# Performance work log

Hardware: AMD Instinct MI355X
Metric: run time of the kernel (lower is better)

The kernel has to match this reference:

```python
import jax, jax.numpy as jnp
import numpy as np

B, C, H, W = 8, 384, 32, 32
NH, DK, DV = 8, 48, 48
CFF = 4 * C
L = H * W
NBIAS = (2 * H - 1) * (2 * W - 1)
LN_EPS = 1e-5


def _relative_indices(height, width):
    # rel_idx[q, k] = (gy_k - gy_q + H) * W + (gx_k - gx_q + W), matching the torch loop
    gy, gx = np.meshgrid(np.arange(height), np.arange(width), indexing='ij')
    gy = gy.ravel(); gx = gx.ravel()
    rel = (gy[None, :] - gy[:, None] + height) * width + (gx[None, :] - gx[:, None] + width)
    return jnp.asarray(rel, dtype=jnp.int64)


def setup_inputs() -> dict:
    key = jax.random.key(0)
    ks = jax.random.split(key, 10)
    s = 0.02  # small init scale
    return {
        'x': jax.random.normal(ks[0], (B, C, H, W), dtype=jnp.float32),
        'gamma': jnp.ones((C,), jnp.float32),
        'beta': jnp.zeros((C,), jnp.float32),
        'Wq': jax.random.normal(ks[1], (NH * DK, C), jnp.float32) * s,
        'Wk': jax.random.normal(ks[2], (NH * DK, C), jnp.float32) * s,
        'Wv': jax.random.normal(ks[3], (NH * DV, C), jnp.float32) * s,
        'Wo': jax.random.normal(ks[4], (C, NH * DV), jnp.float32) * s,
        'bo': jnp.zeros((C,), jnp.float32),
        'rel_bias': jax.random.normal(ks[5], (NH, NBIAS), jnp.float32),
        'fc1_w': jax.random.normal(ks[6], (CFF, C), jnp.float32) * s,
        'fc1_b': jnp.zeros((CFF,), jnp.float32),
        'fc2_w': jax.random.normal(ks[7], (C, CFF), jnp.float32) * s,
        'fc2_b': jnp.zeros((C,), jnp.float32),
        'rel_idx': _relative_indices(H, W),
    }


def reference(x, gamma, beta, Wq, Wk, Wv, Wo, bo, rel_bias,
              fc1_w, fc1_b, fc2_w, fc2_b, rel_idx):
    b, c, h_sp, w_sp = x.shape
    l = h_sp * w_sp
    nh = rel_bias.shape[0]
    dk = Wq.shape[0] // nh
    dv = Wv.shape[0] // nh

    # LayerNorm over channel dim (NHWC), then flatten to tokens [b, l, c]
    t = jnp.transpose(x, (0, 2, 3, 1))
    mu = jnp.mean(t, axis=-1, keepdims=True)
    var = jnp.mean(jnp.square(t - mu), axis=-1, keepdims=True)
    t = (t - mu) / jnp.sqrt(var + LN_EPS) * gamma + beta
    tok = t.reshape(b, l, c)

    q = (tok @ Wq.T).reshape(b, l, nh, dk)
    k = (tok @ Wk.T).reshape(b, l, nh, dk)
    v = (tok @ Wv.T).reshape(b, l, nh, dv)

    # gathered relative position bias: [nh, l, l]
    bias = rel_bias[:, rel_idx]
    # note: original applies NO 1/sqrt(d_k) scaling
    scores = jnp.einsum('blhd,bmhd->bhlm', q, k) + bias[None]
    attn = jax.nn.softmax(scores, axis=-1)
    out = jnp.einsum('bhlm,bmhd->blhd', attn, v).reshape(b, l, nh * dv)
    out = out @ Wo.T + bo  # [b, l, c]
    out = jnp.transpose(out, (0, 2, 1)).reshape(b, c, h_sp, w_sp)

    y = x + out  # attention residual (x_stem = x, no downsampling)

    # FFN: 1x1 convs == per-pixel linear over channels; exact (erf) gelu as torch default
    u = jnp.einsum('bchw,oc->bohw', y, fc1_w) + fc1_b[None, :, None, None]
    u = jax.nn.gelu(u, approximate=False)
    u = jnp.einsum('bchw,oc->bohw', u, fc2_w) + fc2_b[None, :, None, None]
    return y + u
```

## Files before the change

kernel.cpp:

```cpp
#include <hip/hip_runtime.h>
#include <math.h>

#define SL 1024
#define CH 384
#define NHEAD 8
#define DH 48
#define NBIAS 3969
#define NTOK 8192
#define BATCH 8
#define CFF 1536
#define LN_EPS 1e-5f
#define QKVLD 1152
#define HMS 3145728
#define LOG2E 1.4426950408889634f

#define WQKV_OFF 0
#define WO_OFF   442368
#define F1_OFF   589824
#define F2_OFF   1179648
#define WTOT     1769472

typedef float floatx4 __attribute__((ext_vector_type(4)));
typedef short bf16x8 __attribute__((ext_vector_type(8)));

__device__ __forceinline__ unsigned f2bf_u(float f) {
  unsigned u = __float_as_uint(f);
  return (u + 0x7fffu + ((u >> 16) & 1u)) >> 16;
}
__device__ __forceinline__ unsigned pack2(float a, float b) {
  return f2bf_u(a) | (f2bf_u(b) << 16);
}
__device__ __forceinline__ float bf2f(short s) {
  return __uint_as_float(((unsigned)(unsigned short)s) << 16);
}

__device__ __forceinline__ void gload_lds16(const void* g, void* l) {
  __builtin_amdgcn_global_load_lds(
      (const __attribute__((address_space(1))) void*)g,
      (__attribute__((address_space(3))) void*)l, 16, 0, 0);
}

__global__ void k_w2bf(const float* __restrict__ Wq, const float* __restrict__ Wk,
                       const float* __restrict__ Wv, const float* __restrict__ Wo,
                       const float* __restrict__ f1, const float* __restrict__ f2,
                       short* __restrict__ dst) {
  size_t i = ((size_t)blockIdx.x * 256 + threadIdx.x) * 8;
  if (i >= WTOT) return;
  const float* s;
  size_t base;
  if (i < 147456)        { s = Wq; base = 0; }
  else if (i < 294912)   { s = Wk; base = 147456; }
  else if (i < WO_OFF)   { s = Wv; base = 294912; }
  else if (i < F1_OFF)   { s = Wo; base = WO_OFF; }
  else if (i < F2_OFF)   { s = f1; base = F1_OFF; }
  else                   { s = f2; base = F2_OFF; }
  const float4* p = (const float4*)(s + (i - base));
  float4 a = p[0], b = p[1];
  uint4 o;
  o.x = pack2(a.x, a.y); o.y = pack2(a.z, a.w);
  o.z = pack2(b.x, b.y); o.w = pack2(b.z, b.w);
  *(uint4*)(dst + i) = o;
}

__global__ __launch_bounds__(256) void k_ln_fused(
    const float* __restrict__ x, const float* __restrict__ gamma,
    const float* __restrict__ beta, short* __restrict__ tok) {
  __shared__ float sx[32][385];
  int b = blockIdx.y, l0 = blockIdx.x * 32;
  int tid = threadIdx.x;
  const float* xb = x + (size_t)b * CH * SL;
  int cr = tid >> 3, ls = (tid & 7) * 4;
#pragma unroll
  for (int c0 = 0; c0 < CH; c0 += 32) {
    int c = c0 + cr;
    float4 v = *(const float4*)(xb + (size_t)c * SL + l0 + ls);
    sx[ls + 0][c] = v.x; sx[ls + 1][c] = v.y;
    sx[ls + 2][c] = v.z; sx[ls + 3][c] = v.w;
  }
  __syncthreads();
  int tl = tid >> 3, p = tid & 7;
  float vals[48];
  float s = 0.f, q = 0.f;
#pragma unroll
  for (int i = 0; i < 48; i++) {
    float v = sx[tl][p * 48 + i];
    vals[i] = v; s += v; q += v * v;
  }
  s += __shfl_xor(s, 1, 64); q += __shfl_xor(q, 1, 64);
  s += __shfl_xor(s, 2, 64); q += __shfl_xor(q, 2, 64);
  s += __shfl_xor(s, 4, 64); q += __shfl_xor(q, 4, 64);
  float mu = s * (1.0f / CH);
  float rstd = rsqrtf(q * (1.0f / CH) - mu * mu + LN_EPS);
  short* orow = tok + (size_t)(b * SL + l0 + tl) * CH + p * 48;
#pragma unroll
  for (int i = 0; i < 48; i += 2) {
    float a = (vals[i] - mu) * rstd * gamma[p * 48 + i] + beta[p * 48 + i];
    float c = (vals[i + 1] - mu) * rstd * gamma[p * 48 + i + 1] + beta[p * 48 + i + 1];
    *(unsigned*)(orow + i) = pack2(a, c);
  }
}

template <int BM, bool GELU, bool HAS_BIAS, int RES_MODE, int OUT_MODE>
__global__ __launch_bounds__(256) void k_gemm_mfma(
    const short* __restrict__ A, const short* __restrict__ W,
    const float* __restrict__ bias, const float* __restrict__ res,
    float* __restrict__ Cf, short* __restrict__ Cb, float* __restrict__ Ct,
    short* __restrict__ Chm, int N, int K) {
  constexpr int MI = BM / 32;
  constexpr int ASI = BM * 2 / 64;
  __shared__ short As[BM * 64];
  __shared__ short Bs[128 * 64];
  int tid = threadIdx.x;
  int wid = tid >> 6, lane = tid & 63;
  int lanelo = lane & 15, quad = lane >> 4;
  int wm = wid & 1, wn = wid >> 1;
  int m0 = blockIdx.y * BM, n0 = blockIdx.x * 128;

  const short* Aga[ASI];
  short* Ala[ASI];
#pragma unroll
  for (int s = 0; s < ASI; s++) {
    int p = wid * (BM * 2) + s * 64 + lane;
    int row = p >> 3, ch = (p & 7) ^ (row & 7);
    Aga[s] = A + (size_t)(m0 + row) * K + ch * 8;
    Ala[s] = As + (wid * (BM * 2) + s * 64) * 8;
  }
  const short* Bga[4];
  short* Bla[4];
#pragma unroll
  for (int s = 0; s < 4; s++) {
    int p = wid * 256 + s * 64 + lane;
    int row = p >> 3, ch = (p & 7) ^ (row & 7);
    Bga[s] = W + (size_t)(n0 + row) * K + ch * 8;
    Bla[s] = Bs + (wid * 256 + s * 64) * 8;
  }

  floatx4 acc[MI][4];
#pragma unroll
  for (int i = 0; i < MI; i++)
#pragma unroll
    for (int j = 0; j < 4; j++) acc[i][j] = {0.f, 0.f, 0.f, 0.f};

  int x8 = lanelo & 7;
  int ca0 = (quad ^ x8) * 8;
  int ca1 = ((quad + 4) ^ x8) * 8;

  for (int k0 = 0; k0 < K; k0 += 64) {
    __syncthreads();
#pragma unroll
    for (int s = 0; s < ASI; s++) gload_lds16(Aga[s] + k0, Ala[s]);
#pragma unroll
    for (int s = 0; s < 4; s++) gload_lds16(Bga[s] + k0, Bla[s]);
    __syncthreads();
#pragma unroll
    for (int h = 0; h < 2; h++) {
      int co = h ? ca1 : ca0;
      bf16x8 af[MI], bq[4];
#pragma unroll
      for (int i = 0; i < MI; i++)
        af[i] = *(const bf16x8*)&As[(wm * (BM / 2) + i * 16 + lanelo) * 64 + co];
#pragma unroll
      for (int j = 0; j < 4; j++)
        bq[j] = *(const bf16x8*)&Bs[(wn * 64 + j * 16 + lanelo) * 64 + co];
#pragma unroll
      for (int i = 0; i < MI; i++)
#pragma unroll
        for (int j = 0; j < 4; j++)
          acc[i][j] = __builtin_amdgcn_mfma_f32_16x16x32_bf16(af[i], bq[j], acc[i][j], 0, 0, 0);
    }
  }

  int colb = n0 + wn * 64 + lanelo;
  float bvv[4];
#pragma unroll
  for (int j = 0; j < 4; j++) bvv[j] = HAS_BIAS ? bias[colb + j * 16] : 0.0f;
#pragma unroll
  for (int i = 0; i < MI; i++) {
    int r = m0 + wm * (BM / 2) + i * 16 + quad * 4;
    int bb = r >> 10, ll = r & 1023;
#pragma unroll
    for (int j = 0; j < 4; j++) {
      int c = colb + j * 16;
      float4 rv = {0.f, 0.f, 0.f, 0.f};
      if (RES_MODE == 2) rv = *(const float4*)(res + ((size_t)bb * CH + c) * SL + ll);
      float vv[4];
#pragma unroll
      for (int reg = 0; reg < 4; reg++) {
        float v = acc[i][j][reg] + bvv[j];
        if (RES_MODE == 1) v += res[(size_t)(r + reg) * N + c];
        if (RES_MODE == 2) v += (&rv.x)[reg];
        if (GELU) v = 0.5f * v * (1.0f + erff(v * 0.7071067811865476f));
        vv[reg] = v;
      }
      if (OUT_MODE & 1) {
#pragma unroll
        for (int reg = 0; reg < 4; reg++) Cf[(size_t)(r + reg) * N + c] = vv[reg];
      }
      if (OUT_MODE & 2) {
#pragma unroll
        for (int reg = 0; reg < 4; reg++) Cb[(size_t)(r + reg) * N + c] = (short)f2bf_u(vv[reg]);
      }
      if (OUT_MODE & 4) {
        float4 ov = {vv[0], vv[1], vv[2], vv[3]};
        *(float4*)(Ct + ((size_t)bb * CH + c) * SL + ll) = ov;
      }
      if (OUT_MODE & 8) {
        int part = c / 384;
        int rem = c - part * 384;
        int hh = rem / 48, dd = rem - hh * 48;
        short* dst = Chm + (size_t)part * HMS +
                     ((size_t)(bb * NHEAD + hh) * SL + ll) * 48 + dd;
#pragma unroll
        for (int reg = 0; reg < 4; reg++) dst[reg * 48] = (short)f2bf_u(vv[reg]);
      }
    }
  }
}

__global__ __launch_bounds__(256) void k_attn_mfma(
    const short* __restrict__ qh, const short* __restrict__ kh,
    const short* __restrict__ vh, const float* __restrict__ rel_bias,
    short* __restrict__ op, float* __restrict__ ls) {
  __shared__ short QP[128 * 72];
  __shared__ short Ks[64 * 72];
  __shared__ short Vts[48 * 72];
  __shared__ float Bb[640];

  int b = blockIdx.z, h = blockIdx.y;
  int ks = blockIdx.x & 1;
  int l0 = (blockIdx.x >> 1) * 128;
  int ms = ks * 512;
  int tid = threadIdx.x;
  int wid = tid >> 6, lane = tid & 63;
  int lanelo = lane & 15, quad = lane >> 4;
  size_t hb = ((size_t)b * NHEAD + h) * SL;
  const short* kbase = kh + (hb + ms) * 48;
  const short* vbase = vh + (hb + ms) * 48;

  {
    const short* qsrc = qh + (hb + l0) * 48;
#pragma unroll
    for (int s = 0; s < 3; s++) {
      int g = tid + 256 * s;
      int row = g / 6, pos = g - row * 6;
      *(uint4*)&QP[row * 72 + pos * 8] = *(const uint4*)(qsrc + g * 8);
    }
  }
  {
    const float* bsrc = rel_bias + h * NBIAS + (929 - l0 + ms);
    for (int j = tid; j < 640; j += 256) Bb[j] = bsrc[j] * LOG2E;
  }
  for (int z = tid; z < 128 * 8; z += 256) {
    int r = z >> 3, u = z & 7;
    ((unsigned*)&QP[r * 72 + 48])[u] = 0u;
    if (r < 64) ((unsigned*)&Ks[r * 72 + 48])[u] = 0u;
  }
  __syncthreads();

  bf16x8 aq[2][2];
#pragma unroll
  for (int i = 0; i < 2; i++) {
    aq[i][0] = *(const bf16x8*)&QP[(wid * 32 + i * 16 + lanelo) * 72 + quad * 8];
    aq[i][1] = *(const bf16x8*)&QP[(wid * 32 + i * 16 + lanelo) * 72 + 32 + quad * 8];
  }

  floatx4 O[2][3];
#pragma unroll
  for (int i = 0; i < 2; i++)
#pragma unroll
    for (int d = 0; d < 3; d++) O[i][d] = {0.f, 0.f, 0.f, 0.f};
  float lsum[2][4] = {{0.f, 0.f, 0.f, 0.f}, {0.f, 0.f, 0.f, 0.f}};
  int boffL[2];
#pragma unroll
  for (int i = 0; i < 2; i++)
    boffL[i] = 127 - (wid * 32 + i * 16 + quad * 4) + lanelo;

  int kg = 2 * tid;
  int krow = kg / 6, kpos = kg - krow * 6;
  int vmp = tid & 31, vdg = tid >> 5;

  short* Pw = &QP[wid * 32 * 72];

  for (int mt = 0; mt < 512; mt += 64) {
    __syncthreads();
    if (tid < 192) {
      const short* ksrc = kbase + (size_t)mt * 48 + kg * 8;
      *(uint4*)&Ks[krow * 72 + kpos * 8] = *(const uint4*)(ksrc);
      *(uint4*)&Ks[krow * 72 + (kpos + 1) * 8] = *(const uint4*)(ksrc + 8);
      const short* vs = vbase + (size_t)(mt + 2 * vmp) * 48 + vdg * 8;
      union { uint4 u; unsigned short s[8]; } va, vb;
      va.u = *(const uint4*)vs;
      vb.u = *(const uint4*)(vs + 48);
#pragma unroll
      for (int i = 0; i < 8; i++) {
        unsigned pk = (unsigned)va.s[i] | ((unsigned)vb.s[i] << 16);
        *(unsigned*)&Vts[(vdg * 8 + i) * 72 + 2 * vmp] = pk;
      }
    }
    __syncthreads();

    bf16x8 kb[4][2];
#pragma unroll
    for (int nt = 0; nt < 4; nt++) {
      kb[nt][0] = *(const bf16x8*)&Ks[(nt * 16 + lanelo) * 72 + quad * 8];
      kb[nt][1] = *(const bf16x8*)&Ks[(nt * 16 + lanelo) * 72 + 32 + quad * 8];
    }

#pragma unroll
    for (int i = 0; i < 2; i++) {
      floatx4 s[4];
#pragma unroll
      for (int nt = 0; nt < 4; nt++) {
        floatx4 a = {0.f, 0.f, 0.f, 0.f};
        a = __builtin_amdgcn_mfma_f32_16x16x32_bf16(aq[i][0], kb[nt][0], a, 0, 0, 0);
        a = __builtin_amdgcn_mfma_f32_16x16x32_bf16(aq[i][1], kb[nt][1], a, 0, 0, 0);
        s[nt] = a;
      }
#pragma unroll
      for (int nt = 0; nt < 4; nt++) {
        int mo = mt + nt * 16;
#pragma unroll
        for (int reg = 0; reg < 4; reg++) {
          float e = exp2f(fmaf(s[nt][reg], LOG2E, Bb[boffL[i] - reg + mo]));
          lsum[i][reg] += e;
          Pw[(i * 16 + quad * 4 + reg) * 72 + nt * 16 + lanelo] = (short)f2bf_u(e);
        }
      }
    }
    __asm__ volatile("s_waitcnt lgkmcnt(0)" ::: "memory");
    bf16x8 pa[2][2];
#pragma unroll
    for (int i = 0; i < 2; i++) {
      pa[i][0] = *(const bf16x8*)&Pw[(i * 16 + lanelo) * 72 + quad * 8];
      pa[i][1] = *(const bf16x8*)&Pw[(i * 16 + lanelo) * 72 + 32 + quad * 8];
    }
#pragma unroll
    for (int d = 0; d < 3; d++) {
      bf16x8 v0 = *(const bf16x8*)&Vts[(d * 16 + lanelo) * 72 + quad * 8];
      bf16x8 v1 = *(const bf16x8*)&Vts[(d * 16 + lanelo) * 72 + 32 + quad * 8];
#pragma unroll
      for (int i = 0; i < 2; i++) {
        O[i][d] = __builtin_amdgcn_mfma_f32_16x16x32_bf16(pa[i][0], v0, O[i][d], 0, 0, 0);
        O[i][d] = __builtin_amdgcn_mfma_f32_16x16x32_bf16(pa[i][1], v1, O[i][d], 0, 0, 0);
      }
    }
  }

  size_t obase = (size_t)ks * HMS + hb * 48;
  int lsbase = ks * (BATCH * NHEAD * SL) + (int)(hb);
#pragma unroll
  for (int i = 0; i < 2; i++)
#pragma unroll
    for (int reg = 0; reg < 4; reg++) {
      float s = lsum[i][reg];
      s += __shfl_xor(s, 1, 64);
      s += __shfl_xor(s, 2, 64);
      s += __shfl_xor(s, 4, 64);
      s += __shfl_xor(s, 8, 64);
      int q = l0 + wid * 32 + i * 16 + quad * 4 + reg;
      if (lanelo == 0) ls[lsbase + q] = s;
      size_t base = obase + (size_t)q * 48;
      op[base + 0 + lanelo]  = (short)f2bf_u(O[i][0][reg]);
      op[base + 16 + lanelo] = (short)f2bf_u(O[i][1][reg]);
      op[base + 32 + lanelo] = (short)f2bf_u(O[i][2][reg]);
    }
}

#define NROWS 65536
__global__ __launch_bounds__(256) void k_attn_combine(
    const short* __restrict__ op, const float* __restrict__ ls,
    short* __restrict__ ao) {
  int gid = blockIdx.x * 256 + threadIdx.x;
  int row = gid / 6, ch = gid - row * 6;
  float inv = 1.0f / (ls[row] + ls[NROWS + row]);
  bf16x8 va = *(const bf16x8*)(op + (size_t)row * 48 + ch * 8);
  bf16x8 vb = *(const bf16x8*)(op + (size_t)HMS + (size_t)row * 48 + ch * 8);
  int b = row >> 13, h = (row >> 10) & 7, q = row & 1023;
  short* dst = ao + ((size_t)(b << 10) + q) * CH + h * 48 + ch * 8;
  unsigned outw[4];
#pragma unroll
  for (int j = 0; j < 4; j++) {
    float a0 = bf2f(va[2 * j]), a1 = bf2f(va[2 * j + 1]);
    float b0 = bf2f(vb[2 * j]), b1 = bf2f(vb[2 * j + 1]);
    outw[j] = pack2((a0 + b0) * inv, (a1 + b1) * inv);
  }
  *(uint4*)dst = *(uint4*)outw;
}

extern "C" void kernel_launch(void* const* d_in, const int* in_sizes, int n_in,
                              void* d_out, int out_size, void* d_ws, size_t ws_size,
                              hipStream_t stream) {
  const float* x = (const float*)d_in[0];
  const float* gamma = (const float*)d_in[1];
  const float* beta = (const float*)d_in[2];
  const float* Wq = (const float*)d_in[3];
  const float* Wk = (const float*)d_in[4];
  const float* Wv = (const float*)d_in[5];
  const float* Wo = (const float*)d_in[6];
  const float* bo = (const float*)d_in[7];
  const float* rel_bias = (const float*)d_in[8];
  const float* fc1_w = (const float*)d_in[9];
  const float* fc1_b = (const float*)d_in[10];
  const float* fc2_w = (const float*)d_in[11];
  const float* fc2_b = (const float*)d_in[12];
  float* out = (float*)d_out;

  const size_t TOKCH = (size_t)NTOK * CH;
  float* ws_f = (float*)d_ws;
  float* yb = ws_f;
  short* wbf    = (short*)(yb + TOKCH);
  short* tok_bf = wbf + WTOT;
  short* hm     = tok_bf + TOKCH;
  short* ao_bf  = hm + 3 * (size_t)HMS;
  short* yb_bf  = ao_bf + TOKCH;
  short* h1_bf  = yb_bf + TOKCH;
  short* op  = h1_bf;
  float* lsw = (float*)tok_bf;

  k_w2bf<<<WTOT / 8 / 256, 256, 0, stream>>>(Wq, Wk, Wv, Wo, fc1_w, fc2_w, wbf);
  k_ln_fused<<<dim3(SL / 32, BATCH), 256, 0, stream>>>(x, gamma, beta, tok_bf);

  k_gemm_mfma<128, false, false, 0, 8>
      <<<dim3(QKVLD / 128, NTOK / 128), 256, 0, stream>>>(
          tok_bf, wbf + WQKV_OFF, nullptr, nullptr, nullptr, nullptr, nullptr,
          hm, QKVLD, CH);

  k_attn_mfma<<<dim3((SL / 128) * 2, NHEAD, BATCH), 256, 0, stream>>>(
      hm, hm + HMS, hm + 2 * (size_t)HMS, rel_bias, op, lsw);
  k_attn_combine<<<(NROWS * 6) / 256, 256, 0, stream>>>(op, lsw, ao_bf);

  k_gemm_mfma<64, false, true, 2, 3>
      <<<dim3(CH / 128, NTOK / 64), 256, 0, stream>>>(
          ao_bf, wbf + WO_OFF, bo, x, yb, yb_bf, nullptr, nullptr, CH, CH);

  k_gemm_mfma<128, true, true, 0, 2>
      <<<dim3(CFF / 128, NTOK / 128), 256, 0, stream>>>(
          yb_bf, wbf + F1_OFF, fc1_b, nullptr, nullptr, h1_bf, nullptr, nullptr,
          CFF, CH);

  k_gemm_mfma<64, false, true, 1, 4>
      <<<dim3(CH / 128, NTOK / 64), 256, 0, stream>>>(
          h1_bf, wbf + F2_OFF, fc2_b, yb, nullptr, nullptr, out, nullptr, CH, CFF);
}
```

Measured before the change: 223.4 us.

## Restructure attention with pre-swizzled K/V layouts, async LDS double-buffering, register P

The QKV GEMM epilogue now writes K padded to 64 columns with an XOR swizzle and writes V pre-transposed and swizzled, so the attention kernel can stream tiles into LDS with direct global-to-LDS loads into double buffers. The attention kernel drops to 128 threads with 64 query rows per wave. It computes S^T so that exp'd probabilities stay in registers as the B operand, removing the LDS round trip for P. A ones row appended to V lets an extra MFMA produce the softmax row sums, and the output is staged through LDS for coalesced stores. This trades more register pressure and extra MFMA work for less LDS traffic, fewer shuffles and overlap of loads with compute.

```diff
diff --git a/kernel.cpp b/kernel.cpp
--- a/kernel.cpp
+++ b/kernel.cpp
@@ -12,6 +12,8 @@
 #define LN_EPS 1e-5f
 #define QKVLD 1152
 #define HMS 3145728
+#define KHMS 4194304
+#define NROWS 65536
 #define LOG2E 1.4426950408889634f
 
 #define WQKV_OFF 0
@@ -32,6 +34,11 @@
 }
 __device__ __forceinline__ float bf2f(short s) {
   return __uint_as_float(((unsigned)(unsigned short)s) << 16);
+}
+__device__ __forceinline__ unsigned cvtpk(float lo, float hi) {
+  unsigned r;
+  asm("v_cvt_pk_bf16_f32 %0, %1, %2" : "=v"(r) : "v"(lo), "v"(hi));
+  return r;
 }
 
 __device__ __forceinline__ void gload_lds16(const void* g, void* l) {
@@ -105,7 +112,8 @@
     const short* __restrict__ A, const short* __restrict__ W,
     const float* __restrict__ bias, const float* __restrict__ res,
     float* __restrict__ Cf, short* __restrict__ Cb, float* __restrict__ Ct,
-    short* __restrict__ Chm, int N, int K) {
+    short* __restrict__ Chm, short* __restrict__ Ckm, short* __restrict__ Cvm,
+    int N, int K) {
   constexpr int MI = BM / 32;
   constexpr int ASI = BM * 2 / 64;
   __shared__ short As[BM * 64];
@@ -208,165 +216,193 @@
         int part = c / 384;
         int rem = c - part * 384;
         int hh = rem / 48, dd = rem - hh * 48;
-        short* dst = Chm + (size_t)part * HMS +
-                     ((size_t)(bb * NHEAD + hh) * SL + ll) * 48 + dd;
-#pragma unroll
-        for (int reg = 0; reg < 4; reg++) dst[reg * 48] = (short)f2bf_u(vv[reg]);
-      }
-    }
-  }
-}
-
-__global__ __launch_bounds__(256) void k_attn_mfma(
+        int bhh = bb * NHEAD + hh;
+        if (part == 0) {
+          short* dst = Chm + ((size_t)bhh * SL + ll) * 48 + dd;
+#pragma unroll
+          for (int reg = 0; reg < 4; reg++) dst[reg * 48] = (short)f2bf_u(vv[reg]);
+        } else if (part == 1) {
+          short* dst = Ckm + ((size_t)bhh * SL + ll) * 64;
+#pragma unroll
+          for (int reg = 0; reg < 4; reg++) {
+            int mm = (ll + reg) & 7;
+            dst[reg * 64 + (dd & 7) + (((dd >> 3) ^ mm) << 3)] = (short)f2bf_u(vv[reg]);
+            if (dd < 16)
+              dst[reg * 64 + (dd & 7) + ((((dd + 48) >> 3) ^ mm) << 3)] = 0;
+          }
+        } else {
+          int kk = ll & 63;
+          int sig = ((kk >> 2) & 3) * 8 + ((kk >> 4) & 1) * 4 + (kk >> 5) * 32;
+          int mcol = (ll & ~63) + (sig ^ ((dd & 7) << 3));
+          uint2 pk = {pack2(vv[0], vv[1]), pack2(vv[2], vv[3])};
+          *(uint2*)(Cvm + ((size_t)bhh * 48 + dd) * SL + mcol) = pk;
+        }
+      }
+    }
+  }
+}
+
+__global__ __launch_bounds__(128) void k_attn_mfma(
     const short* __restrict__ qh, const short* __restrict__ kh,
-    const short* __restrict__ vh, const float* __restrict__ rel_bias,
+    const short* __restrict__ vt, const float* __restrict__ rel_bias,
     short* __restrict__ op, float* __restrict__ ls) {
   __shared__ short QP[128 * 72];
-  __shared__ short Ks[64 * 72];
-  __shared__ short Vts[48 * 72];
-  __shared__ float Bb[640];
-
+  __shared__ short Ks[2][64 * 64];
+  __shared__ short Vts[2][64 * 64];
+  float4* Bt = (float4*)QP;
+
+  int ksp = blockIdx.x & 1;
+  int l0 = (blockIdx.x >> 1) * 128;
+  int ms = ksp * 512;
   int b = blockIdx.z, h = blockIdx.y;
-  int ks = blockIdx.x & 1;
-  int l0 = (blockIdx.x >> 1) * 128;
-  int ms = ks * 512;
   int tid = threadIdx.x;
   int wid = tid >> 6, lane = tid & 63;
   int lanelo = lane & 15, quad = lane >> 4;
-  size_t hb = ((size_t)b * NHEAD + h) * SL;
-  const short* kbase = kh + (hb + ms) * 48;
-  const short* vbase = vh + (hb + ms) * 48;
-
-  {
-    const short* qsrc = qh + (hb + l0) * 48;
-#pragma unroll
-    for (int s = 0; s < 3; s++) {
-      int g = tid + 256 * s;
-      int row = g / 6, pos = g - row * 6;
-      *(uint4*)&QP[row * 72 + pos * 8] = *(const uint4*)(qsrc + g * 8);
-    }
-  }
+  int bh = b * NHEAD + h;
+  size_t hb = (size_t)bh * SL;
+  const short* kbase = kh + ((size_t)bh * SL + ms) * 64;
+  const short* vtbase = vt + (size_t)bh * 48 * SL + ms;
+
+  bf16x8 aq[4][2];
+  bf16x8 zf = {0, 0, 0, 0, 0, 0, 0, 0};
+#pragma unroll
+  for (int qi = 0; qi < 4; qi++) {
+    const short* qsrc = qh + (hb + l0 + wid * 64 + qi * 16 + lanelo) * 48;
+    aq[qi][0] = *(const bf16x8*)(qsrc + quad * 8);
+    aq[qi][1] = (quad < 2) ? *(const bf16x8*)(qsrc + 32 + quad * 8) : zf;
+  }
+
   {
     const float* bsrc = rel_bias + h * NBIAS + (929 - l0 + ms);
-    for (int j = tid; j < 640; j += 256) Bb[j] = bsrc[j] * LOG2E;
-  }
-  for (int z = tid; z < 128 * 8; z += 256) {
-    int r = z >> 3, u = z & 7;
-    ((unsigned*)&QP[r * 72 + 48])[u] = 0u;
-    if (r < 64) ((unsigned*)&Ks[r * 72 + 48])[u] = 0u;
+    for (int j = tid; j < 640; j += 128) {
+      float4 t;
+      t.x = bsrc[j] * LOG2E;     t.y = bsrc[j + 1] * LOG2E;
+      t.z = bsrc[j + 2] * LOG2E; t.w = bsrc[j + 3] * LOG2E;
+      Bt[j] = t;
+    }
+  }
+  for (int z = tid; z < 1024; z += 128) {
+    int bi = z >> 9, o = z & 511;
+    int row = 48 + (o >> 5), colu = o & 31;
+    ((unsigned*)&Vts[bi][row * 64])[colu] = (row == 48) ? 0x3F803F80u : 0u;
+  }
+#pragma unroll
+  for (int c = 0; c < 4; c++)
+    gload_lds16(kbase + (size_t)(c * 128 + tid) * 8, &Ks[0][(c * 128 + wid * 64) * 8]);
+#pragma unroll
+  for (int c = 0; c < 3; c++) {
+    int g = c * 128 + tid;
+    gload_lds16(vtbase + (size_t)(g >> 3) * SL + (g & 7) * 8,
+                &Vts[0][(c * 128 + wid * 64) * 8]);
   }
   __syncthreads();
 
-  bf16x8 aq[2][2];
-#pragma unroll
-  for (int i = 0; i < 2; i++) {
-    aq[i][0] = *(const bf16x8*)&QP[(wid * 32 + i * 16 + lanelo) * 72 + quad * 8];
-    aq[i][1] = *(const bf16x8*)&QP[(wid * 32 + i * 16 + lanelo) * 72 + 32 + quad * 8];
-  }
-
-  floatx4 O[2][3];
-#pragma unroll
-  for (int i = 0; i < 2; i++)
-#pragma unroll
-    for (int d = 0; d < 3; d++) O[i][d] = {0.f, 0.f, 0.f, 0.f};
-  float lsum[2][4] = {{0.f, 0.f, 0.f, 0.f}, {0.f, 0.f, 0.f, 0.f}};
-  int boffL[2];
-#pragma unroll
-  for (int i = 0; i < 2; i++)
-    boffL[i] = 127 - (wid * 32 + i * 16 + quad * 4) + lanelo;
-
-  int kg = 2 * tid;
-  int krow = kg / 6, kpos = kg - krow * 6;
-  int vmp = tid & 31, vdg = tid >> 5;
-
-  short* Pw = &QP[wid * 32 * 72];
-
+  floatx4 O[3][4];
+  floatx4 O3[4];
+#pragma unroll
+  for (int qi = 0; qi < 4; qi++) {
+#pragma unroll
+    for (int dt = 0; dt < 3; dt++) O[dt][qi] = {0.f, 0.f, 0.f, 0.f};
+    O3[qi] = {0.f, 0.f, 0.f, 0.f};
+  }
+  int swz = (lanelo & 7) << 3;
+  int base00 = 127 + quad * 4 - wid * 64 - lanelo;
+
+  int cur = 0;
   for (int mt = 0; mt < 512; mt += 64) {
-    __syncthreads();
-    if (tid < 192) {
-      const short* ksrc = kbase + (size_t)mt * 48 + kg * 8;
-      *(uint4*)&Ks[krow * 72 + kpos * 8] = *(const uint4*)(ksrc);
-      *(uint4*)&Ks[krow * 72 + (kpos + 1) * 8] = *(const uint4*)(ksrc + 8);
-      const short* vs = vbase + (size_t)(mt + 2 * vmp) * 48 + vdg * 8;
-      union { uint4 u; unsigned short s[8]; } va, vb;
-      va.u = *(const uint4*)vs;
-      vb.u = *(const uint4*)(vs + 48);
-#pragma unroll
-      for (int i = 0; i < 8; i++) {
-        unsigned pk = (unsigned)va.s[i] | ((unsigned)vb.s[i] << 16);
-        *(unsigned*)&Vts[(vdg * 8 + i) * 72 + 2 * vmp] = pk;
-      }
-    }
-    __syncthreads();
-
-    bf16x8 kb[4][2];
+    if (mt + 64 < 512) {
+      int nxt = cur ^ 1, mtn = mt + 64;
+#pragma unroll
+      for (int c = 0; c < 4; c++)
+        gload_lds16(kbase + (size_t)mtn * 64 + (size_t)(c * 128 + tid) * 8,
+                    &Ks[nxt][(c * 128 + wid * 64) * 8]);
+#pragma unroll
+      for (int c = 0; c < 3; c++) {
+        int g = c * 128 + tid;
+        gload_lds16(vtbase + (size_t)(g >> 3) * SL + mtn + (g & 7) * 8,
+                    &Vts[nxt][(c * 128 + wid * 64) * 8]);
+      }
+    }
+
+    bf16x8 kb[4][2], vf[3][2], vo[2];
 #pragma unroll
     for (int nt = 0; nt < 4; nt++) {
-      kb[nt][0] = *(const bf16x8*)&Ks[(nt * 16 + lanelo) * 72 + quad * 8];
-      kb[nt][1] = *(const bf16x8*)&Ks[(nt * 16 + lanelo) * 72 + 32 + quad * 8];
-    }
-
-#pragma unroll
-    for (int i = 0; i < 2; i++) {
-      floatx4 s[4];
+      kb[nt][0] = *(const bf16x8*)&Ks[cur][(nt * 16 + lanelo) * 64 + ((quad * 8) ^ swz)];
+      kb[nt][1] = *(const bf16x8*)&Ks[cur][(nt * 16 + lanelo) * 64 + ((32 + quad * 8) ^ swz)];
+    }
+#pragma unroll
+    for (int dt = 0; dt < 3; dt++) {
+      vf[dt][0] = *(const bf16x8*)&Vts[cur][(dt * 16 + lanelo) * 64 + ((quad * 8) ^ swz)];
+      vf[dt][1] = *(const bf16x8*)&Vts[cur][(dt * 16 + lanelo) * 64 + ((32 + quad * 8) ^ swz)];
+    }
+    vo[0] = *(const bf16x8*)&Vts[cur][(48 + lanelo) * 64 + ((quad * 8) ^ swz)];
+    vo[1] = *(const bf16x8*)&Vts[cur][(48 + lanelo) * 64 + ((32 + quad * 8) ^ swz)];
+
+    float4 bv[7];
+    int b0 = base00 + mt;
+#pragma unroll
+    for (int t = 0; t < 7; t++) bv[t] = Bt[b0 + 16 * t - 48];
+
+#pragma unroll
+    for (int qi = 0; qi < 4; qi++) {
+      floatx4 sc[4];
 #pragma unroll
       for (int nt = 0; nt < 4; nt++) {
         floatx4 a = {0.f, 0.f, 0.f, 0.f};
-        a = __builtin_amdgcn_mfma_f32_16x16x32_bf16(aq[i][0], kb[nt][0], a, 0, 0, 0);
-        a = __builtin_amdgcn_mfma_f32_16x16x32_bf16(aq[i][1], kb[nt][1], a, 0, 0, 0);
-        s[nt] = a;
-      }
+        a = __builtin_amdgcn_mfma_f32_16x16x32_bf16(kb[nt][0], aq[qi][0], a, 0, 0, 0);
+        a = __builtin_amdgcn_mfma_f32_16x16x32_bf16(kb[nt][1], aq[qi][1], a, 0, 0, 0);
+        sc[nt] = a;
+      }
+      union U8 { unsigned u[4]; bf16x8 v; } pb0, pb1;
 #pragma unroll
       for (int nt = 0; nt < 4; nt++) {
-        int mo = mt + nt * 16;
-#pragma unroll
-        for (int reg = 0; reg < 4; reg++) {
-          float e = exp2f(fmaf(s[nt][reg], LOG2E, Bb[boffL[i] - reg + mo]));
-          lsum[i][reg] += e;
-          Pw[(i * 16 + quad * 4 + reg) * 72 + nt * 16 + lanelo] = (short)f2bf_u(e);
-        }
-      }
-    }
-    __asm__ volatile("s_waitcnt lgkmcnt(0)" ::: "memory");
-    bf16x8 pa[2][2];
-#pragma unroll
-    for (int i = 0; i < 2; i++) {
-      pa[i][0] = *(const bf16x8*)&Pw[(i * 16 + lanelo) * 72 + quad * 8];
-      pa[i][1] = *(const bf16x8*)&Pw[(i * 16 + lanelo) * 72 + 32 + quad * 8];
-    }
-#pragma unroll
-    for (int d = 0; d < 3; d++) {
-      bf16x8 v0 = *(const bf16x8*)&Vts[(d * 16 + lanelo) * 72 + quad * 8];
-      bf16x8 v1 = *(const bf16x8*)&Vts[(d * 16 + lanelo) * 72 + 32 + quad * 8];
-#pragma unroll
-      for (int i = 0; i < 2; i++) {
-        O[i][d] = __builtin_amdgcn_mfma_f32_16x16x32_bf16(pa[i][0], v0, O[i][d], 0, 0, 0);
-        O[i][d] = __builtin_amdgcn_mfma_f32_16x16x32_bf16(pa[i][1], v1, O[i][d], 0, 0, 0);
-      }
-    }
-  }
-
-  size_t obase = (size_t)ks * HMS + hb * 48;
-  int lsbase = ks * (BATCH * NHEAD * SL) + (int)(hb);
-#pragma unroll
-  for (int i = 0; i < 2; i++)
-#pragma unroll
-    for (int reg = 0; reg < 4; reg++) {
-      float s = lsum[i][reg];
-      s += __shfl_xor(s, 1, 64);
-      s += __shfl_xor(s, 2, 64);
-      s += __shfl_xor(s, 4, 64);
-      s += __shfl_xor(s, 8, 64);
-      int q = l0 + wid * 32 + i * 16 + quad * 4 + reg;
-      if (lanelo == 0) ls[lsbase + q] = s;
-      size_t base = obase + (size_t)q * 48;
-      op[base + 0 + lanelo]  = (short)f2bf_u(O[i][0][reg]);
-      op[base + 16 + lanelo] = (short)f2bf_u(O[i][1][reg]);
-      op[base + 32 + lanelo] = (short)f2bf_u(O[i][2][reg]);
-    }
-}
-
-#define NROWS 65536
+        float4 bb = bv[nt - qi + 3];
+        float e0 = __builtin_amdgcn_exp2f(fmaf(sc[nt][0], LOG2E, bb.x));
+        float e1 = __builtin_amdgcn_exp2f(fmaf(sc[nt][1], LOG2E, bb.y));
+        float e2 = __builtin_amdgcn_exp2f(fmaf(sc[nt][2], LOG2E, bb.z));
+        float e3 = __builtin_amdgcn_exp2f(fmaf(sc[nt][3], LOG2E, bb.w));
+        unsigned p01 = cvtpk(e0, e1), p23 = cvtpk(e2, e3);
+        if (nt == 0)      { pb0.u[0] = p01; pb0.u[1] = p23; }
+        else if (nt == 1) { pb0.u[2] = p01; pb0.u[3] = p23; }
+        else if (nt == 2) { pb1.u[0] = p01; pb1.u[1] = p23; }
+        else              { pb1.u[2] = p01; pb1.u[3] = p23; }
+      }
+#pragma unroll
+      for (int dt = 0; dt < 3; dt++) {
+        O[dt][qi] = __builtin_amdgcn_mfma_f32_16x16x32_bf16(vf[dt][0], pb0.v, O[dt][qi], 0, 0, 0);
+        O[dt][qi] = __builtin_amdgcn_mfma_f32_16x16x32_bf16(vf[dt][1], pb1.v, O[dt][qi], 0, 0, 0);
+      }
+      O3[qi] = __builtin_amdgcn_mfma_f32_16x16x32_bf16(vo[0], pb0.v, O3[qi], 0, 0, 0);
+      O3[qi] = __builtin_amdgcn_mfma_f32_16x16x32_bf16(vo[1], pb1.v, O3[qi], 0, 0, 0);
+    }
+    __syncthreads();
+    cur ^= 1;
+  }
+
+  if (quad == 0) {
+#pragma unroll
+    for (int qi = 0; qi < 4; qi++)
+      ls[(size_t)ksp * NROWS + hb + l0 + wid * 64 + qi * 16 + lanelo] = O3[qi][0];
+  }
+#pragma unroll
+  for (int dt = 0; dt < 3; dt++)
+#pragma unroll
+    for (int qi = 0; qi < 4; qi++) {
+      uint2 wv = {cvtpk(O[dt][qi][0], O[dt][qi][1]),
+                  cvtpk(O[dt][qi][2], O[dt][qi][3])};
+      *(uint2*)&QP[(wid * 64 + qi * 16 + lanelo) * 72 + dt * 16 + quad * 4] = wv;
+    }
+  __asm__ volatile("s_waitcnt lgkmcnt(0)" ::: "memory");
+#pragma unroll
+  for (int c = 0; c < 6; c++) {
+    int g = c * 64 + lane;
+    int rl = g / 6, pos = g - rl * 6;
+    int rowl = wid * 64 + rl;
+    uint4 val = *(const uint4*)&QP[rowl * 72 + pos * 8];
+    *(uint4*)(op + (size_t)ksp * HMS + (hb + l0 + rowl) * 48 + pos * 8) = val;
+  }
+}
+
 __global__ __launch_bounds__(256) void k_attn_combine(
     const short* __restrict__ op, const float* __restrict__ ls,
     short* __restrict__ ao) {
@@ -410,11 +446,13 @@
   float* yb = ws_f;
   short* wbf    = (short*)(yb + TOKCH);
   short* tok_bf = wbf + WTOT;
-  short* hm     = tok_bf + TOKCH;
-  short* ao_bf  = hm + 3 * (size_t)HMS;
+  short* qhm    = tok_bf + TOKCH;
+  short* khm    = qhm + HMS;
+  short* vtm    = khm + KHMS;
+  short* ao_bf  = vtm + HMS;
   short* yb_bf  = ao_bf + TOKCH;
   short* h1_bf  = yb_bf + TOKCH;
-  short* op  = h1_bf;
+  short* opw = h1_bf;
   float* lsw = (float*)tok_bf;
 
   k_w2bf<<<WTOT / 8 / 256, 256, 0, stream>>>(Wq, Wk, Wv, Wo, fc1_w, fc2_w, wbf);
@@ -423,22 +461,24 @@
   k_gemm_mfma<128, false, false, 0, 8>
       <<<dim3(QKVLD / 128, NTOK / 128), 256, 0, stream>>>(
           tok_bf, wbf + WQKV_OFF, nullptr, nullptr, nullptr, nullptr, nullptr,
-          hm, QKVLD, CH);
-
-  k_attn_mfma<<<dim3((SL / 128) * 2, NHEAD, BATCH), 256, 0, stream>>>(
-      hm, hm + HMS, hm + 2 * (size_t)HMS, rel_bias, op, lsw);
-  k_attn_combine<<<(NROWS * 6) / 256, 256, 0, stream>>>(op, lsw, ao_bf);
+          qhm, khm, vtm, QKVLD, CH);
+
+  k_attn_mfma<<<dim3((SL / 128) * 2, NHEAD, BATCH), 128, 0, stream>>>(
+      qhm, khm, vtm, rel_bias, opw, lsw);
+  k_attn_combine<<<(NROWS * 6) / 256, 256, 0, stream>>>(opw, lsw, ao_bf);
 
   k_gemm_mfma<64, false, true, 2, 3>
       <<<dim3(CH / 128, NTOK / 64), 256, 0, stream>>>(
-          ao_bf, wbf + WO_OFF, bo, x, yb, yb_bf, nullptr, nullptr, CH, CH);
+          ao_bf, wbf + WO_OFF, bo, x, yb, yb_bf, nullptr, nullptr, nullptr,
+          nullptr, CH, CH);
 
   k_gemm_mfma<128, true, true, 0, 2>
       <<<dim3(CFF / 128, NTOK / 128), 256, 0, stream>>>(
           yb_bf, wbf + F1_OFF, fc1_b, nullptr, nullptr, h1_bf, nullptr, nullptr,
-          CFF, CH);
+          nullptr, nullptr, CFF, CH);
 
   k_gemm_mfma<64, false, true, 1, 4>
       <<<dim3(CH / 128, NTOK / 64), 256, 0, stream>>>(
-          h1_bf, wbf + F2_OFF, fc2_b, yb, nullptr, nullptr, out, nullptr, CH, CFF);
-}
+          h1_bf, wbf + F2_OFF, fc2_b, yb, nullptr, nullptr, out, nullptr,
+          nullptr, nullptr, CH, CFF);
+}
```

After: 217.5 us. 2.6% less time.
